# Kernel tuning notes

Hardware: AMD Instinct MI355X
Metric: run time of the kernel (lower is better)

## Reference

```python
import jax, jax.numpy as jnp
import numpy as np
from jax import lax

BN_EPS = 1e-5


def ternary_quantize(x):
    # thresholds from global max/min, split range into thirds
    mx, mn = jnp.max(x), jnp.min(x)
    lo = mn + (mx - mn) / 3
    hi = mx - (mx - mn) / 3
    return jnp.where(x < lo, -1.0, jnp.where(x > hi, 1.0, 0.0)).astype(x.dtype)


def noised_tri_conv(x, w):
    # w: [O, I, 3, 3]; bias=False in BasicBlock
    tw = w - jnp.mean(w)
    tq = ternary_quantize(tw)
    out = lax.conv_general_dilated(
        x, tq, window_strides=(1, 1), padding=((1, 1), (1, 1)),
        dimension_numbers=('NCHW', 'OIHW', 'NCHW'))
    # noised_forward: per-pixel conv of a 1x1 patch with padding=1 ->
    # only the center tap of the 3x3 kernel contributes; generated noise
    # weights are unused in the original code (faithful reproduction);
    # result is detached in torch.
    center = tq[:, :, 1, 1]  # [O, I]
    extra = lax.stop_gradient(jnp.einsum('bchw,oc->bohw', x, center))
    return out + extra


def batch_norm_train(x, gamma, beta):
    mean = jnp.mean(x, axis=(0, 2, 3), keepdims=True)
    var = jnp.var(x, axis=(0, 2, 3), keepdims=True)  # biased, as torch BN
    xhat = (x - mean) * lax.rsqrt(var + BN_EPS)
    return xhat * gamma[None, :, None, None] + beta[None, :, None, None]


def setup_inputs() -> dict:
    key = jax.random.key(0)
    k = jax.random.split(key, 7)
    C = 256
    x = jax.random.normal(k[0], (16, C, 56, 56), dtype=jnp.float32)
    w1 = jax.random.normal(k[1], (C, C, 3, 3), dtype=jnp.float32) * 0.05
    w2 = jax.random.normal(k[2], (C, C, 3, 3), dtype=jnp.float32) * 0.05
    g1 = jax.random.uniform(k[3], (C,), dtype=jnp.float32, minval=0.5, maxval=1.5)
    b1 = jax.random.normal(k[4], (C,), dtype=jnp.float32) * 0.1
    g2 = jax.random.uniform(k[5], (C,), dtype=jnp.float32, minval=0.5, maxval=1.5)
    b2 = jax.random.normal(k[6], (C,), dtype=jnp.float32) * 0.1
    return {'x': x, 'w1': w1, 'w2': w2, 'g1': g1, 'b1': b1, 'g2': g2, 'b2': b2}


def reference(x, w1, w2, g1, b1, g2, b2):
    out1 = noised_tri_conv(x, w1)
    out1 = batch_norm_train(out1, g1, b1)
    out1 = jax.nn.relu(out1)
    out2 = noised_tri_conv(out1, w2)
    out2 = batch_norm_train(out2, g2, b2)
    return jax.nn.relu(out1 + out2)
```

## Files before the change

### kernel.cpp

```cpp
#include <hip/hip_runtime.h>

typedef __bf16 bf16;
typedef __bf16 bf16x8 __attribute__((ext_vector_type(8)));
typedef float f32x4 __attribute__((ext_vector_type(4)));

#define NIMG 16
#define CCH 256
#define HH 56
#define HP 58
#define NBLK (NIMG * 14)
#define NPART 896
#define NPOSV (NIMG * HH * HH)
#define WELEMS 589824

typedef const __attribute__((address_space(1))) void* gas1_t;
typedef __attribute__((address_space(3))) void* las3_t;

__device__ __forceinline__ void gload16(const void* g, void* l) {
  __builtin_amdgcn_global_load_lds((gas1_t)g, (las3_t)l, 16, 0, 0);
}


__global__ __launch_bounds__(256) void w_partial(const float* __restrict__ w1,
                                                 const float* __restrict__ w2,
                                                 double* __restrict__ psum,
                                                 float* __restrict__ pmn,
                                                 float* __restrict__ pmx) {
  int b = blockIdx.x;
  int lb = b & 127;
  const float* w = (b >> 7) ? w2 : w1;
  int t = threadIdx.x;
  double s = 0.0;
  float mn = 3.4028235e38f, mx = -3.4028235e38f;
  for (int i = lb * 4608 + t; i < (lb + 1) * 4608; i += 256) {
    float v = w[i];
    s += (double)v;
    mn = fminf(mn, v);
    mx = fmaxf(mx, v);
  }
  __shared__ double sd[256];
  __shared__ float smn[256], smx[256];
  sd[t] = s; smn[t] = mn; smx[t] = mx;
  __syncthreads();
  for (int st = 128; st > 0; st >>= 1) {
    if (t < st) {
      sd[t] += sd[t + st];
      smn[t] = fminf(smn[t], smn[t + st]);
      smx[t] = fmaxf(smx[t], smx[t + st]);
    }
    __syncthreads();
  }
  if (t == 0) { psum[b] = sd[0]; pmn[b] = smn[0]; pmx[b] = smx[0]; }
}

__global__ void w_finalize(const double* __restrict__ psum,
                           const float* __restrict__ pmn,
                           const float* __restrict__ pmx,
                           float* __restrict__ wq) {
  int t = threadIdx.x;
  if (t < 2) {
    double s = 0.0;
    float mn = 3.4028235e38f, mx = -3.4028235e38f;
    for (int b = t * 128; b < (t + 1) * 128; b++) {
      s += psum[b];
      mn = fminf(mn, pmn[b]);
      mx = fmaxf(mx, pmx[b]);
    }
    float mean = (float)(s / (double)WELEMS);
    float tmn = mn - mean, tmx = mx - mean;
    float d = (tmx - tmn) / 3.0f;
    wq[t * 4 + 0] = mean;
    wq[t * 4 + 1] = tmn + d;
    wq[t * 4 + 2] = tmx - d;
  }
}

__global__ __launch_bounds__(256) void w_quant(const float* __restrict__ w1,
                                               const float* __restrict__ w2,
                                               const float* __restrict__ wq,
                                               bf16* __restrict__ btf1,
                                               bf16* __restrict__ btf2) {
  int bid = blockIdx.x;
  int widx = bid / 2304;
  const float* w = widx ? w2 : w1;
  bf16* bt = widx ? btf2 : btf1;
  float mean = wq[widx * 4], lo = wq[widx * 4 + 1], hi = wq[widx * 4 + 2];
  int e = (bid % 2304) * 256 + threadIdx.x;
  int ki = e & 7;
  int l = (e >> 3) & 63;
  int frag = e >> 9;
  int ob = frag & 15;
  int rest = frag >> 4;
  int kk = rest & 1;
  int scc = rest >> 1;
  int cc = scc & 3;
  int s = scc >> 2;
  int o = ob * 16 + (l & 15);
  int c = cc * 64 + kk * 32 + (l >> 4) * 8 + ki;
  float tv = w[(size_t)o * 2304 + c * 9 + s] - mean;
  float q = tv < lo ? -1.f : (tv > hi ? 1.f : 0.f);
  if (s == 4) q *= 2.f;
  bt[e] = (bf16)q;
}

__global__ __launch_bounds__(256) void pad_convert(const float* __restrict__ x,
                                                   bf16* __restrict__ xpad) {
  int bid = blockIdx.x;
  int cchunk = bid & 3;
  int hp = (bid >> 2) % HP;
  int n = (bid >> 2) / HP;
  int t = threadIdx.x;
  bf16* orow = xpad + (size_t)(n * HP + hp) * HP * CCH;
  if (hp == 0 || hp == HP - 1) {
    for (int j = t; j < HP * 64; j += 256)
      orow[(size_t)(j >> 6) * CCH + cchunk * 64 + (j & 63)] = (bf16)0.f;
    return;
  }
  int h = hp - 1;
  __shared__ float tile[HH * 65];
  const float* xb = x + ((size_t)n * CCH + cchunk * 64) * (HH * HH) + h * HH;
  for (int j = t; j < 64 * 64; j += 256) {
    int w = j & 63, cc = j >> 6;
    if (w < HH) tile[w * 65 + cc] = xb[(size_t)cc * (HH * HH) + w];
  }
  __syncthreads();
  for (int j = t; j < HP * 64; j += 256) {
    int wp = j >> 6, cc = j & 63;
    float v = (wp == 0 || wp == HP - 1) ? 0.f : tile[(wp - 1) * 65 + cc];
    orow[(size_t)wp * CCH + cchunk * 64 + cc] = (bf16)v;
  }
}

template <int MODE>
__global__ __launch_bounds__(512, 2) void conv_gemm(const bf16* __restrict__ xpad,
                                                    const bf16* __restrict__ btf,
                                                    float* __restrict__ outr,
                                                    float* __restrict__ part,
                                                    const bf16* __restrict__ v1pad,
                                                    const float* __restrict__ bnp,
                                                    float* __restrict__ outf,
                                                    bf16* __restrict__ outb) {
  __shared__ __align__(16) char smem[116736];
  const int t = threadIdx.x;
  const int lane = t & 63, wv = t >> 6;
  const int wm = wv >> 2, wn = wv & 3;
  const int g = lane >> 4, li = lane & 15;
  const int bid = blockIdx.x;
  const int n = bid / 14, h0 = (bid % 14) * 4;

  f32x4 acc[8][4];
#pragma unroll
  for (int i = 0; i < 8; i++)
#pragma unroll
    for (int j = 0; j < 4; j++) acc[i][j] = f32x4{0.f, 0.f, 0.f, 0.f};

  auto stageA = [&](int cc, int b) {
#pragma unroll
    for (int i = 0; i < 6; ++i) {
      int idx = wv + i * 8;
      int rr = idx >> 3, po = idx & 7;
      int pp = po * 8 + (lane >> 3);
      int gs = (lane & 7) ^ (lane >> 3);
      const bf16* src = xpad + ((size_t)(n * HP + h0 + rr) * HP + pp) * CCH + cc * 64 + gs * 8;
      gload16(src, smem + b * 49152 + rr * 8192 + po * 1024 + lane * 16);
    }
  };

  auto loadB = [&](bf16x8 (&dst)[4], int s, int cc, int kk) {
#pragma unroll
    for (int f = 0; f < 4; ++f) {
      size_t fragidx = (size_t)(((s * 4 + cc) * 2 + kk) * 16 + wn * 4 + f);
      dst[f] = *(const bf16x8*)(btf + fragidx * 512 + lane * 8);
    }
  };

  auto compute_half = [&](const char* Ab, int half, int dh, int dw, int kk,
                          const bf16x8 (&bx)[4]) {
    bf16x8 a[4];
    int rr = 2 * wm + half + dh;
#pragma unroll
    for (int pc = 0; pc < 4; ++pc) {
      int p = pc * 16 + li + dw;
      int sl = (kk * 4 + g) ^ (p & 7);
      a[pc] = *(const bf16x8*)(Ab + rr * 8192 + p * 128 + sl * 16);
    }
#pragma unroll
    for (int pc = 0; pc < 4; ++pc)
#pragma unroll
      for (int fn = 0; fn < 4; ++fn)
        acc[half * 4 + pc][fn] =
          __builtin_amdgcn_mfma_f32_16x16x32_bf16(a[pc], bx[fn], acc[half * 4 + pc][fn], 0, 0, 0);
  };

  stageA(0, 0);
  bf16x8 bS[2][4];
  bf16x8 bB[4];
  loadB(bS[0], 0, 0, 0);
  __syncthreads();

#pragma unroll
  for (int cc = 0; cc < 4; ++cc) {
    const char* Ab = smem + (cc & 1) * 49152;
    if (cc < 3) stageA(cc + 1, (cc + 1) & 1);
#pragma unroll
    for (int s = 0; s < 9; ++s) {
      const int dh = s / 3, dw = s % 3;
      const int cur = (cc * 9 + s) & 1, nxt = cur ^ 1;
      if (s < 8) loadB(bS[nxt], s + 1, cc, 0);
      else if (cc < 3) loadB(bS[nxt], 0, cc + 1, 0);
      loadB(bB, s, cc, 1);
      __builtin_amdgcn_sched_barrier(0);
      __builtin_amdgcn_s_setprio(1);
      compute_half(Ab, 0, dh, dw, 0, bS[cur]);
      compute_half(Ab, 1, dh, dw, 0, bS[cur]);
      compute_half(Ab, 0, dh, dw, 1, bB);
      compute_half(Ab, 1, dh, dw, 1, bB);
      __builtin_amdgcn_s_setprio(0);
    }
    __syncthreads();
  }

  if (MODE == 0 || MODE == 1 || MODE == 3) {
    float so[2][4] = {{0.f,0.f,0.f,0.f},{0.f,0.f,0.f,0.f}};
    float qo[2][4] = {{0.f,0.f,0.f,0.f},{0.f,0.f,0.f,0.f}};
#pragma unroll
    for (int fm = 0; fm < 8; ++fm) {
      const int rl = fm >> 2, pc = fm & 3;
      const size_t rowoff = (size_t)(n * HH + h0 + 2 * wm + rl) * HH * CCH;
#pragma unroll
      for (int r = 0; r < 4; ++r) {
        int w = pc * 16 + g * 4 + r;
        if (w < HH) {
#pragma unroll
          for (int fn = 0; fn < 4; ++fn) {
            float v = acc[fm][fn][r];
            so[rl][fn] += v;
            qo[rl][fn] += v * v;
            if (MODE == 0) outr[rowoff + (size_t)w * CCH + wn * 64 + fn * 16 + li] = v;
            if (MODE == 3) outb[rowoff + (size_t)w * CCH + wn * 64 + fn * 16 + li] = (bf16)v;
          }
        }
      }
    }
#pragma unroll
    for (int rl = 0; rl < 2; ++rl)
#pragma unroll
      for (int fn = 0; fn < 4; ++fn) {
        so[rl][fn] += __shfl_xor(so[rl][fn], 16);
        so[rl][fn] += __shfl_xor(so[rl][fn], 32);
        qo[rl][fn] += __shfl_xor(qo[rl][fn], 16);
        qo[rl][fn] += __shfl_xor(qo[rl][fn], 32);
      }
    if (g == 0) {
#pragma unroll
      for (int rl = 0; rl < 2; ++rl)
#pragma unroll
        for (int fn = 0; fn < 4; ++fn) {
          int o = wn * 64 + fn * 16 + lane;
          size_t prow = (size_t)(bid * 4 + 2 * wm + rl);
          part[(prow * CCH + o) * 2 + 0] = so[rl][fn];
          part[(prow * CCH + o) * 2 + 1] = qo[rl][fn];
        }
    }
  } else {
    float sc[4], bi[4];
#pragma unroll
    for (int fn = 0; fn < 4; ++fn) {
      int o = wn * 64 + fn * 16 + li;
      sc[fn] = bnp[o * 2];
      bi[fn] = bnp[o * 2 + 1];
    }
    float* fsm = (float*)smem;
    const int TS = 3648;
    for (int rl = 0; rl < 2; ++rl) {
      __syncthreads();
      const int row = h0 + 2 * wm + rl;
#pragma unroll
      for (int pc = 0; pc < 4; ++pc) {
        const int fm = rl * 4 + pc;
#pragma unroll
        for (int r = 0; r < 4; ++r) {
          int w = pc * 16 + g * 4 + r;
          if (w < HH) {
#pragma unroll
            for (int fn = 0; fn < 4; ++fn) {
              int o_loc = fn * 16 + li;
              fsm[wv * TS + w * 65 + o_loc] = acc[fm][fn][r] * sc[fn] + bi[fn];
            }
          }
        }
      }
      const bf16* v1row = v1pad + ((size_t)(n * HP + row + 1) * HP + 1) * CCH + wn * 64;
      for (int i = lane; i < HH * 8; i += 64) {
        int w = i >> 3, og = i & 7;
        bf16x8 v1v = *(const bf16x8*)(v1row + (size_t)w * CCH + og * 8);
        float* tp = &fsm[wv * TS + w * 65 + og * 8];
#pragma unroll
        for (int q = 0; q < 8; ++q) {
          float v = tp[q] + (float)v1v[q];
          tp[q] = v > 0.f ? v : 0.f;
        }
      }
      __syncthreads();
#pragma unroll
      for (int tl = 0; tl < 8; ++tl) {
        int wmt = tl >> 2, wnt = tl & 3;
        int orow = h0 + 2 * wmt + rl;
        for (int j = t; j < 4096; j += 512) {
          int oo = j >> 6, w = j & 63;
          if (w < HH)
            outf[(((size_t)n * CCH + wnt * 64 + oo) * HH + orow) * HH + w] = fsm[tl * TS + w * 65 + oo];
        }
      }
    }
  }
}

__global__ __launch_bounds__(256) void fuse2(const bf16* __restrict__ raw,
                                             const bf16* __restrict__ v1pad,
                                             const float* __restrict__ bnp,
                                             float* __restrict__ out) {
  __shared__ float tile[HH * 261];
  int bid = blockIdx.x;
  int n = bid / HH, h = bid % HH;
  int t = threadIdx.x;
  const bf16* rrow = raw + (size_t)(n * HH + h) * HH * CCH;
  const bf16* vrow = v1pad + ((size_t)(n * HP + h + 1) * HP + 1) * CCH;
  for (int j = t; j < HH * 32; j += 256) {
    int w = j >> 5, cg = j & 31;
    bf16x8 r8 = *(const bf16x8*)(rrow + (size_t)w * CCH + cg * 8);
    bf16x8 v8 = *(const bf16x8*)(vrow + (size_t)w * CCH + cg * 8);
    float* tp = &tile[w * 261 + cg * 8];
#pragma unroll
    for (int q = 0; q < 8; ++q) {
      int c = cg * 8 + q;
      float v = (float)r8[q] * bnp[c * 2] + bnp[c * 2 + 1] + (float)v8[q];
      tp[q] = v > 0.f ? v : 0.f;
    }
  }
  __syncthreads();
  float* ob = out + (((size_t)n * CCH) * HH + h) * HH;
  for (int j = t; j < CCH * 64; j += 256) {
    int w = j & 63, c = j >> 6;
    if (w < HH) ob[(size_t)c * (HH * HH) + w] = tile[w * 261 + c];
  }
}

__global__ __launch_bounds__(256) void bn_reduce1(const float* __restrict__ part,
                                                  float* __restrict__ part2) {
  int t = threadIdx.x, b = blockIdx.x;
  float s = 0.f, q = 0.f;
  for (int r = b * 28; r < (b + 1) * 28; r++) {
    s += part[((size_t)r * CCH + t) * 2 + 0];
    q += part[((size_t)r * CCH + t) * 2 + 1];
  }
  part2[((size_t)b * CCH + t) * 2 + 0] = s;
  part2[((size_t)b * CCH + t) * 2 + 1] = q;
}

__global__ __launch_bounds__(256) void bn_reduce2(const float* __restrict__ part2,
                                                  const float* __restrict__ gamma,
                                                  const float* __restrict__ beta,
                                                  float* __restrict__ params) {
  int t = threadIdx.x;
  float s = 0.f, q = 0.f;
  for (int b = 0; b < 32; b++) {
    s += part2[((size_t)b * CCH + t) * 2 + 0];
    q += part2[((size_t)b * CCH + t) * 2 + 1];
  }
  const float inv = 1.f / (float)NPOSV;
  float mean = s * inv;
  float var = q * inv - mean * mean;
  float sc = gamma[t] / sqrtf(var + 1e-5f);
  params[t * 2 + 0] = sc;
  params[t * 2 + 1] = beta[t] - mean * sc;
}

__global__ __launch_bounds__(256) void bn_apply_pad(const float* __restrict__ raw,
                                                    const float* __restrict__ params,
                                                    bf16* __restrict__ xpad) {
  int bid = blockIdx.x;
  int hp = bid % HP;
  int n = bid / HP;
  int t = threadIdx.x;
  bf16* orow = xpad + (size_t)(n * HP + hp) * HP * CCH;
  if (hp == 0 || hp == HP - 1) {
    for (int j = t; j < HP * CCH; j += 256) orow[j] = (bf16)0.f;
    return;
  }
  float sc = params[t * 2], bi = params[t * 2 + 1];
  const float* irow = raw + (size_t)(n * HH + (hp - 1)) * HH * CCH;
  for (int j = t; j < HP * CCH; j += 256) {
    int wp = j >> 8;
    float v = 0.f;
    if (wp >= 1 && wp <= HH) {
      v = irow[(size_t)(wp - 1) * CCH + t] * sc + bi;
      v = v > 0.f ? v : 0.f;
    }
    orow[j] = (bf16)v;
  }
}


extern "C" void kernel_launch(void* const* d_in, const int* in_sizes, int n_in,
                              void* d_out, int out_size, void* d_ws, size_t ws_size,
                              hipStream_t stream) {
  const float* x  = (const float*)d_in[0];
  const float* w1 = (const float*)d_in[1];
  const float* w2 = (const float*)d_in[2];
  const float* g1 = (const float*)d_in[3];
  const float* b1 = (const float*)d_in[4];
  const float* g2 = (const float*)d_in[5];
  const float* b2 = (const float*)d_in[6];
  float* out = (float*)d_out;
  char* ws = (char*)d_ws;

  constexpr size_t O_BT1  = 0;
  constexpr size_t O_BT2  = O_BT1 + 1179648;
  constexpr size_t O_XPAD = O_BT2 + 1179648;
  constexpr size_t O_PART = O_XPAD + (size_t)NIMG * HP * HP * CCH * 2 + 65536;
  constexpr size_t O_PSUM = O_PART + (size_t)NPART * CCH * 2 * 4;
  constexpr size_t O_PMN  = O_PSUM + 2048;
  constexpr size_t O_PMX  = O_PMN + 1024;
  constexpr size_t O_WQ   = O_PMX + 1024;
  constexpr size_t O_BNP1 = O_WQ + 256;
  constexpr size_t O_BNP2 = O_BNP1 + 2048;
  constexpr size_t O_PART2 = O_BNP2 + 2048;
  constexpr size_t O_OUT2RAW = O_PART2 + 65536;
  constexpr size_t NEED_BIG = O_OUT2RAW + (size_t)NPOSV * CCH * 2 + 65536;

  bf16* bt1 = (bf16*)(ws + O_BT1);
  bf16* bt2 = (bf16*)(ws + O_BT2);
  bf16* xpad = (bf16*)(ws + O_XPAD);
  bf16* out1pad = (bf16*)(ws + O_XPAD);
  float* part = (float*)(ws + O_PART);
  double* psum = (double*)(ws + O_PSUM);
  float* pmn = (float*)(ws + O_PMN);
  float* pmx = (float*)(ws + O_PMX);
  float* wq = (float*)(ws + O_WQ);
  float* bnp1 = (float*)(ws + O_BNP1);
  float* bnp2 = (float*)(ws + O_BNP2);
  float* part2 = (float*)(ws + O_PART2);
  bf16* out2raw = (bf16*)(ws + O_OUT2RAW);
  float* out1raw = out;

  w_partial<<<256, 256, 0, stream>>>(w1, w2, psum, pmn, pmx);
  w_finalize<<<1, 64, 0, stream>>>(psum, pmn, pmx, wq);
  w_quant<<<4608, 256, 0, stream>>>(w1, w2, wq, bt1, bt2);
  pad_convert<<<NIMG * HP * 4, 256, 0, stream>>>(x, xpad);
  conv_gemm<0><<<NBLK, 512, 0, stream>>>(xpad, bt1, out1raw, part, nullptr, nullptr, nullptr, nullptr);
  bn_reduce1<<<32, 256, 0, stream>>>(part, part2);
  bn_reduce2<<<1, 256, 0, stream>>>(part2, g1, b1, bnp1);
  bn_apply_pad<<<NIMG * HP, 256, 0, stream>>>(out1raw, bnp1, out1pad);
  if (ws_size >= NEED_BIG) {
    conv_gemm<3><<<NBLK, 512, 0, stream>>>(out1pad, bt2, nullptr, part, nullptr, nullptr, nullptr, out2raw);
    bn_reduce1<<<32, 256, 0, stream>>>(part, part2);
    bn_reduce2<<<1, 256, 0, stream>>>(part2, g2, b2, bnp2);
    fuse2<<<NIMG * HH, 256, 0, stream>>>(out2raw, out1pad, bnp2, out);
  } else {
    conv_gemm<1><<<NBLK, 512, 0, stream>>>(out1pad, bt2, nullptr, part, nullptr, nullptr, nullptr, nullptr);
    bn_reduce1<<<32, 256, 0, stream>>>(part, part2);
    bn_reduce2<<<1, 256, 0, stream>>>(part2, g2, b2, bnp2);
    conv_gemm<2><<<NBLK, 512, 0, stream>>>(out1pad, bt2, nullptr, nullptr, out1pad, bnp2, out, nullptr);
  }
}
```

Before: 210.5 us.

## Store conv1 raw output in bf16, vectorize pad/fuse kernels, swizzle block order

The first conv now writes its raw output as bf16 instead of fp32 (MODE 3), and the BN-apply kernel reads bf16 with 8-wide vector loads and stores. pad_convert and fuse2 are restructured to use one block per row covering all channels, with float4 global accesses and bf16x8 stores through a transposed shared tile. conv_gemm blocks are remapped with an XCD-style swizzle so that neighbouring rows land on the same chiplet. These changes cut global memory traffic in the elementwise kernels and may improve L2 locality, at the cost of rounding the intermediate conv1 result to bf16.

```diff
diff --git a/kernel.cpp b/kernel.cpp
--- a/kernel.cpp
+++ b/kernel.cpp
@@ -106,35 +106,42 @@
 __global__ __launch_bounds__(256) void pad_convert(const float* __restrict__ x,
                                                    bf16* __restrict__ xpad) {
   int bid = blockIdx.x;
-  int cchunk = bid & 3;
-  int hp = (bid >> 2) % HP;
-  int n = (bid >> 2) / HP;
+  int hp = bid % HP;
+  int n = bid / HP;
   int t = threadIdx.x;
   bf16* orow = xpad + (size_t)(n * HP + hp) * HP * CCH;
+  bf16x8 z;
+#pragma unroll
+  for (int q = 0; q < 8; ++q) z[q] = (bf16)0.f;
   if (hp == 0 || hp == HP - 1) {
-    for (int j = t; j < HP * 64; j += 256)
-      orow[(size_t)(j >> 6) * CCH + cchunk * 64 + (j & 63)] = (bf16)0.f;
+    for (int j = t; j < HP * 32; j += 256)
+      *(bf16x8*)(orow + (size_t)(j >> 5) * CCH + (j & 31) * 8) = z;
     return;
   }
-  int h = hp - 1;
-  __shared__ float tile[HH * 65];
-  const float* xb = x + ((size_t)n * CCH + cchunk * 64) * (HH * HH) + h * HH;
-  for (int j = t; j < 64 * 64; j += 256) {
-    int w = j & 63, cc = j >> 6;
-    if (w < HH) tile[w * 65 + cc] = xb[(size_t)cc * (HH * HH) + w];
+  __shared__ float tile[CCH * 57];
+  const float* xb = x + (size_t)n * CCH * (HH * HH) + (size_t)(hp - 1) * HH;
+  for (int j = t; j < CCH * 14; j += 256) {
+    int c = j / 14, wq = j % 14;
+    float4 v = *(const float4*)(xb + (size_t)c * (HH * HH) + wq * 4);
+    float* tp = &tile[c * 57 + wq * 4];
+    tp[0] = v.x; tp[1] = v.y; tp[2] = v.z; tp[3] = v.w;
   }
   __syncthreads();
-  for (int j = t; j < HP * 64; j += 256) {
-    int wp = j >> 6, cc = j & 63;
-    float v = (wp == 0 || wp == HP - 1) ? 0.f : tile[(wp - 1) * 65 + cc];
-    orow[(size_t)wp * CCH + cchunk * 64 + cc] = (bf16)v;
+  const int cg = t & 31;
+  for (int j = t; j < HP * 32; j += 256) {
+    int wp = j >> 5;
+    bf16x8 ov = z;
+    if (wp >= 1 && wp <= HH) {
+#pragma unroll
+      for (int q = 0; q < 8; ++q) ov[q] = (bf16)tile[(cg * 8 + q) * 57 + (wp - 1)];
+    }
+    *(bf16x8*)(orow + (size_t)wp * CCH + cg * 8) = ov;
   }
 }
 
 template <int MODE>
 __global__ __launch_bounds__(512, 2) void conv_gemm(const bf16* __restrict__ xpad,
                                                     const bf16* __restrict__ btf,
-                                                    float* __restrict__ outr,
                                                     float* __restrict__ part,
                                                     const bf16* __restrict__ v1pad,
                                                     const float* __restrict__ bnp,
@@ -145,7 +152,8 @@
   const int lane = t & 63, wv = t >> 6;
   const int wm = wv >> 2, wn = wv & 3;
   const int g = lane >> 4, li = lane & 15;
-  const int bid = blockIdx.x;
+  const int rawbid = blockIdx.x;
+  const int bid = (rawbid & 7) * (NBLK / 8) + (rawbid >> 3);
   const int n = bid / 14, h0 = (bid % 14) * 4;
 
   f32x4 acc[8][4];
@@ -220,7 +228,7 @@
     __syncthreads();
   }
 
-  if (MODE == 0 || MODE == 1 || MODE == 3) {
+  if (MODE == 1 || MODE == 3) {
     float so[2][4] = {{0.f,0.f,0.f,0.f},{0.f,0.f,0.f,0.f}};
     float qo[2][4] = {{0.f,0.f,0.f,0.f},{0.f,0.f,0.f,0.f}};
 #pragma unroll
@@ -236,7 +244,6 @@
             float v = acc[fm][fn][r];
             so[rl][fn] += v;
             qo[rl][fn] += v * v;
-            if (MODE == 0) outr[rowoff + (size_t)w * CCH + wn * 64 + fn * 16 + li] = v;
             if (MODE == 3) outb[rowoff + (size_t)w * CCH + wn * 64 + fn * 16 + li] = (bf16)v;
           }
         }
@@ -320,29 +327,36 @@
                                              const bf16* __restrict__ v1pad,
                                              const float* __restrict__ bnp,
                                              float* __restrict__ out) {
-  __shared__ float tile[HH * 261];
+  __shared__ float tile[CCH * 57];
   int bid = blockIdx.x;
   int n = bid / HH, h = bid % HH;
   int t = threadIdx.x;
   const bf16* rrow = raw + (size_t)(n * HH + h) * HH * CCH;
   const bf16* vrow = v1pad + ((size_t)(n * HP + h + 1) * HP + 1) * CCH;
+  const int cg = t & 31;
+  float sc[8], bi[8];
+#pragma unroll
+  for (int q = 0; q < 8; ++q) {
+    sc[q] = bnp[(cg * 8 + q) * 2];
+    bi[q] = bnp[(cg * 8 + q) * 2 + 1];
+  }
   for (int j = t; j < HH * 32; j += 256) {
-    int w = j >> 5, cg = j & 31;
+    int w = j >> 5;
     bf16x8 r8 = *(const bf16x8*)(rrow + (size_t)w * CCH + cg * 8);
     bf16x8 v8 = *(const bf16x8*)(vrow + (size_t)w * CCH + cg * 8);
-    float* tp = &tile[w * 261 + cg * 8];
 #pragma unroll
     for (int q = 0; q < 8; ++q) {
-      int c = cg * 8 + q;
-      float v = (float)r8[q] * bnp[c * 2] + bnp[c * 2 + 1] + (float)v8[q];
-      tp[q] = v > 0.f ? v : 0.f;
+      float v = (float)r8[q] * sc[q] + bi[q] + (float)v8[q];
+      tile[(cg * 8 + q) * 57 + w] = v > 0.f ? v : 0.f;
     }
   }
   __syncthreads();
-  float* ob = out + (((size_t)n * CCH) * HH + h) * HH;
-  for (int j = t; j < CCH * 64; j += 256) {
-    int w = j & 63, c = j >> 6;
-    if (w < HH) ob[(size_t)c * (HH * HH) + w] = tile[w * 261 + c];
+  float* ob = out + (size_t)n * CCH * (HH * HH) + (size_t)h * HH;
+  for (int j = t; j < CCH * 14; j += 256) {
+    int c = j / 14, wq = j % 14;
+    const float* tp = &tile[c * 57 + wq * 4];
+    float4 v = {tp[0], tp[1], tp[2], tp[3]};
+    *(float4*)(ob + (size_t)c * (HH * HH) + wq * 4) = v;
   }
 }
 
@@ -376,28 +390,41 @@
   params[t * 2 + 1] = beta[t] - mean * sc;
 }
 
-__global__ __launch_bounds__(256) void bn_apply_pad(const float* __restrict__ raw,
-                                                    const float* __restrict__ params,
-                                                    bf16* __restrict__ xpad) {
+__global__ __launch_bounds__(256) void bn_apply_b(const bf16* __restrict__ rawb,
+                                                  const float* __restrict__ params,
+                                                  bf16* __restrict__ xpad) {
   int bid = blockIdx.x;
   int hp = bid % HP;
   int n = bid / HP;
   int t = threadIdx.x;
   bf16* orow = xpad + (size_t)(n * HP + hp) * HP * CCH;
+  bf16x8 z;
+#pragma unroll
+  for (int q = 0; q < 8; ++q) z[q] = (bf16)0.f;
   if (hp == 0 || hp == HP - 1) {
-    for (int j = t; j < HP * CCH; j += 256) orow[j] = (bf16)0.f;
+    for (int j = t; j < HP * 32; j += 256)
+      *(bf16x8*)(orow + (size_t)(j >> 5) * CCH + (j & 31) * 8) = z;
     return;
   }
-  float sc = params[t * 2], bi = params[t * 2 + 1];
-  const float* irow = raw + (size_t)(n * HH + (hp - 1)) * HH * CCH;
-  for (int j = t; j < HP * CCH; j += 256) {
-    int wp = j >> 8;
-    float v = 0.f;
+  const int cg = t & 31, ws8 = t >> 5;
+  float sc[8], bi[8];
+#pragma unroll
+  for (int q = 0; q < 8; ++q) {
+    sc[q] = params[(cg * 8 + q) * 2];
+    bi[q] = params[(cg * 8 + q) * 2 + 1];
+  }
+  const bf16* rrow = rawb + (size_t)(n * HH + (hp - 1)) * HH * CCH;
+  for (int wp = ws8; wp < HP; wp += 8) {
+    bf16x8 ov = z;
     if (wp >= 1 && wp <= HH) {
-      v = irow[(size_t)(wp - 1) * CCH + t] * sc + bi;
-      v = v > 0.f ? v : 0.f;
-    }
-    orow[j] = (bf16)v;
+      bf16x8 r8 = *(const bf16x8*)(rrow + (size_t)(wp - 1) * CCH + cg * 8);
+#pragma unroll
+      for (int q = 0; q < 8; ++q) {
+        float v = (float)r8[q] * sc[q] + bi[q];
+        ov[q] = (bf16)(v > 0.f ? v : 0.f);
+      }
+    }
+    *(bf16x8*)(orow + (size_t)wp * CCH + cg * 8) = ov;
   }
 }
 
@@ -442,25 +469,25 @@
   float* bnp2 = (float*)(ws + O_BNP2);
   float* part2 = (float*)(ws + O_PART2);
   bf16* out2raw = (bf16*)(ws + O_OUT2RAW);
-  float* out1raw = out;
+  bf16* out1rawb = (bf16*)d_out;
 
   w_partial<<<256, 256, 0, stream>>>(w1, w2, psum, pmn, pmx);
   w_finalize<<<1, 64, 0, stream>>>(psum, pmn, pmx, wq);
   w_quant<<<4608, 256, 0, stream>>>(w1, w2, wq, bt1, bt2);
-  pad_convert<<<NIMG * HP * 4, 256, 0, stream>>>(x, xpad);
-  conv_gemm<0><<<NBLK, 512, 0, stream>>>(xpad, bt1, out1raw, part, nullptr, nullptr, nullptr, nullptr);
+  pad_convert<<<NIMG * HP, 256, 0, stream>>>(x, xpad);
+  conv_gemm<3><<<NBLK, 512, 0, stream>>>(xpad, bt1, part, nullptr, nullptr, nullptr, out1rawb);
   bn_reduce1<<<32, 256, 0, stream>>>(part, part2);
   bn_reduce2<<<1, 256, 0, stream>>>(part2, g1, b1, bnp1);
-  bn_apply_pad<<<NIMG * HP, 256, 0, stream>>>(out1raw, bnp1, out1pad);
+  bn_apply_b<<<NIMG * HP, 256, 0, stream>>>(out1rawb, bnp1, out1pad);
   if (ws_size >= NEED_BIG) {
-    conv_gemm<3><<<NBLK, 512, 0, stream>>>(out1pad, bt2, nullptr, part, nullptr, nullptr, nullptr, out2raw);
+    conv_gemm<3><<<NBLK, 512, 0, stream>>>(out1pad, bt2, part, nullptr, nullptr, nullptr, out2raw);
     bn_reduce1<<<32, 256, 0, stream>>>(part, part2);
     bn_reduce2<<<1, 256, 0, stream>>>(part2, g2, b2, bnp2);
     fuse2<<<NIMG * HH, 256, 0, stream>>>(out2raw, out1pad, bnp2, out);
   } else {
-    conv_gemm<1><<<NBLK, 512, 0, stream>>>(out1pad, bt2, nullptr, part, nullptr, nullptr, nullptr, nullptr);
+    conv_gemm<1><<<NBLK, 512, 0, stream>>>(out1pad, bt2, part, nullptr, nullptr, nullptr, nullptr);
     bn_reduce1<<<32, 256, 0, stream>>>(part, part2);
     bn_reduce2<<<1, 256, 0, stream>>>(part2, g2, b2, bnp2);
-    conv_gemm<2><<<NBLK, 512, 0, stream>>>(out1pad, bt2, nullptr, nullptr, out1pad, bnp2, out, nullptr);
-  }
-}
+    conv_gemm<2><<<NBLK, 512, 0, stream>>>(out1pad, bt2, nullptr, out1pad, bnp2, out, nullptr);
+  }
+}
```

Result: faster. 192.0 us (-8.8%).
